# Kernel tuning notes

Hardware: AMD Instinct MI355X
Metric: run time of the kernel (lower is better)

The kernel has to match this reference:

```python
import jax, jax.numpy as jnp
import numpy as np

B, L, D, S = 8, 512, 64, 8


def setup_inputs() -> dict:
    key = jax.random.key(0)
    ks = jax.random.split(key, 8)
    return {
        "lstm1": jax.random.normal(ks[0], (B, L, D), dtype=jnp.float32),
        "lstm2": jax.random.normal(ks[1], (B, L, D), dtype=jnp.float32),
        "W": jax.random.normal(ks[2], (S, D, D), dtype=jnp.float32) * 0.1,
        "V": jax.random.normal(ks[3], (S, 2 * D), dtype=jnp.float32) * 0.1,
        "b": jax.random.normal(ks[4], (S,), dtype=jnp.float32) * 0.1,
        "W_g": jax.random.normal(ks[5], (S, 2 * D), dtype=jnp.float32) * 0.1,
        "b_g": jax.random.normal(ks[6], (S,), dtype=jnp.float32) * 0.1,
        "u": jax.random.normal(ks[7], (1, S), dtype=jnp.float32) * 0.1,
    }


def reference(lstm1, lstm2, W, V, b, W_g, b_g, u):
    # lstm1/lstm2: (B, L, D). Pairwise slot (i, j) pairs lstm1[:, i] with lstm2[:, j].
    d = lstm1.shape[-1]
    # Bilinear tensor-network score: x1_i W_s x2_j -> (B, L, L, S)
    result_w = jnp.einsum('bid,sde,bje->bijs', lstm1, W, lstm2)
    # concat(x1_i, x2_j) @ V^T decomposed to avoid materializing (B,L,L,2D)
    v1 = jnp.einsum('bid,sd->bis', lstm1, V[:, :d])[:, :, None, :]   # (B,L,1,S)
    v2 = jnp.einsum('bjd,sd->bjs', lstm2, V[:, d:])[:, None, :, :]   # (B,1,L,S)
    result_v = v1 + v2                                               # (B,L,L,S)
    g1 = jnp.einsum('bid,sd->bis', lstm1, W_g[:, :d])[:, :, None, :]
    g2 = jnp.einsum('bjd,sd->bjs', lstm2, W_g[:, d:])[:, None, :, :]
    gate = jax.nn.sigmoid(g1 + g2 + b_g)                             # (B,L,L,S)
    result_final = gate * result_w + (1.0 - gate) * jax.nn.sigmoid(result_v) + b
    # Reduce slices with u (shape (1,S)) -> (B,L,L), then add singleton channel dim.
    out = jnp.einsum('bijs,ks->bijk', result_final, u)[..., 0]
    return out[:, None, :, :]  # (B, 1, L, L)
```

## Files before the change

### kernel.cpp

```cpp
#include <hip/hip_runtime.h>
#include <math.h>

typedef float f32x4 __attribute__((ext_vector_type(4)));
typedef short bf16x8 __attribute__((ext_vector_type(8)));

namespace {
constexpr int kB = 8, kL = 512, kD = 64, kS = 8;
constexpr int LP = 72;
constexpr size_t SCL_OFF = 0;
constexpr size_t WT_OFF  = (size_t)4 * 8 * 8 * 512 * 4;
}

__device__ __forceinline__ unsigned short f2bf(float f) {
    unsigned u = __float_as_uint(f);
    u += 0x7FFFu + ((u >> 16) & 1u);
    return (unsigned short)(u >> 16);
}
__device__ __forceinline__ unsigned pk2(float lo, float hi) {
    return (unsigned)f2bf(lo) | ((unsigned)f2bf(hi) << 16);
}

__global__ __launch_bounds__(256) void grn_prep(
    const float* __restrict__ lstm1, const float* __restrict__ lstm2,
    const float* __restrict__ W, const float* __restrict__ V,
    const float* __restrict__ Wg, unsigned char* __restrict__ ws)
{
    float* scl = (float*)(ws + SCL_OFF);
    unsigned short* wt = (unsigned short*)(ws + WT_OFF);
    const int tid = threadIdx.x;
    if (blockIdx.x < 8) {
        const int s = blockIdx.x;
        __shared__ float wsm[64][68];
        const float* pw = W + s * 4096;
        const int row = tid >> 2, c0 = (tid & 3) * 16;
        #pragma unroll
        for (int q = 0; q < 4; q++)
            *(float4*)&wsm[row][c0 + q * 4] = *(const float4*)(pw + row * 64 + c0 + q * 4);
        __syncthreads();
        const int e = tid >> 2, d0 = (tid & 3) * 16;
        unsigned wd[8];
        #pragma unroll
        for (int q = 0; q < 8; q++)
            wd[q] = pk2(wsm[d0 + 2 * q][e], wsm[d0 + 2 * q + 1][e]);
        unsigned short* dst = wt + s * 4096 + e * 64 + d0;
        uint4 a = {wd[0], wd[1], wd[2], wd[3]};
        uint4 c = {wd[4], wd[5], wd[6], wd[7]};
        *(uint4*)(dst) = a;
        *(uint4*)(dst + 8) = c;
    } else {
        const int rb = blockIdx.x - 8;
        const int b = rb >> 3, r0 = (rb & 7) * 64;
        const int kind = tid & 3, row = r0 + (tid >> 2);
        const float* x = (kind < 2 ? lstm1 : lstm2) + ((size_t)b * kL + row) * kD;
        float xr[64];
        #pragma unroll
        for (int q = 0; q < 16; q++)
            *(float4*)&xr[q * 4] = *(const float4*)(x + q * 4);
        const float* vb = (kind & 1 ? Wg : V) + ((kind >> 1) ? kD : 0);
        #pragma unroll
        for (int s = 0; s < kS; s++) {
            const float* vec = vb + s * 2 * kD;
            float a = 0.f;
            #pragma unroll
            for (int q = 0; q < 16; q++) {
                const float4 vv = *(const float4*)(vec + q * 4);
                a = fmaf(vv.x, xr[q * 4 + 0], a);
                a = fmaf(vv.y, xr[q * 4 + 1], a);
                a = fmaf(vv.z, xr[q * 4 + 2], a);
                a = fmaf(vv.w, xr[q * 4 + 3], a);
            }
            scl[(((size_t)kind * 8 + b) * 8 + s) * 512 + row] = a;
        }
    }
}

__global__ __launch_bounds__(256) void grn_fusedm(
    const float* __restrict__ lstm1, const float* __restrict__ lstm2,
    const float* __restrict__ bS, const float* __restrict__ bg,
    const float* __restrict__ u, const unsigned char* __restrict__ ws,
    float* __restrict__ out)
{
    const float* sclw = (const float*)(ws + SCL_OFF);
    const unsigned short* wt = (const unsigned short*)(ws + WT_OFF);
    const int jt = blockIdx.x, it = blockIdx.y, b = blockIdx.z;
    __shared__ __align__(16) unsigned short x1t[64][LP];
    __shared__ __align__(16) unsigned short x2t[64][LP];
    __shared__ __align__(16) unsigned short wbuf[2][64][LP];
    __shared__ __align__(16) unsigned short ts[2][64][LP];
    __shared__ float scl[4][kS][64];
    const int tid = threadIdx.x;
    {
        const float* p1 = lstm1 + ((size_t)b * kL + it * 64) * kD;
        const float* p2 = lstm2 + ((size_t)b * kL + jt * 64) * kD;
        const int row = tid >> 2, c0 = (tid & 3) * 16;
        unsigned w1[8], w2[8];
        #pragma unroll
        for (int q = 0; q < 4; q++) {
            const float4 a = *(const float4*)(p1 + row * 64 + c0 + q * 4);
            const float4 c = *(const float4*)(p2 + row * 64 + c0 + q * 4);
            w1[q * 2] = pk2(a.x, a.y); w1[q * 2 + 1] = pk2(a.z, a.w);
            w2[q * 2] = pk2(c.x, c.y); w2[q * 2 + 1] = pk2(c.z, c.w);
        }
        uint4 a0 = {w1[0], w1[1], w1[2], w1[3]}, a1 = {w1[4], w1[5], w1[6], w1[7]};
        uint4 c0v = {w2[0], w2[1], w2[2], w2[3]}, c1 = {w2[4], w2[5], w2[6], w2[7]};
        *(uint4*)&x1t[row][c0] = a0; *(uint4*)&x1t[row][c0 + 8] = a1;
        *(uint4*)&x2t[row][c0] = c0v; *(uint4*)&x2t[row][c0 + 8] = c1;
    }
    {
        #pragma unroll
        for (int k = 0; k < 2; k++) {
            const int q = tid + k * 256;
            *(uint4*)&wbuf[0][q >> 3][(q & 7) * 8] = *(const uint4*)(wt + q * 8);
        }
    }
    {
        const int p0 = tid * 8, kind = p0 >> 9, rem = p0 & 511, s = rem >> 6, cc = rem & 63;
        const int base = (kind < 2 ? it : jt) * 64;
        const float* g = sclw + (((size_t)kind * 8 + b) * 8 + s) * 512 + base + cc;
        *(float4*)&scl[kind][s][cc] = *(const float4*)g;
        *(float4*)&scl[kind][s][cc + 4] = *(const float4*)(g + 4);
    }
    __syncthreads();
    const int lane = tid & 63, w = tid >> 6;
    const int wm = w >> 1, wn = w & 1;
    const int fr = lane & 15, fh = lane >> 4;
    bf16x8 A1[2][2], Bf[2][2];
    #pragma unroll
    for (int mb = 0; mb < 2; mb++)
        #pragma unroll
        for (int kb = 0; kb < 2; kb++)
            A1[mb][kb] = *(const bf16x8*)&x1t[wm * 32 + mb * 16 + fr][fh * 8 + kb * 32];
    #pragma unroll
    for (int nb = 0; nb < 2; nb++)
        #pragma unroll
        for (int kb = 0; kb < 2; kb++)
            Bf[nb][kb] = *(const bf16x8*)&x2t[wn * 32 + nb * 16 + fr][fh * 8 + kb * 32];
    uint4 wreg0 = *(const uint4*)(wt + 4096 + tid * 8);
    uint4 wreg1 = *(const uint4*)(wt + 4096 + (tid + 256) * 8);

    float bias_c = 0.f;
    #pragma unroll
    for (int s = 0; s < kS; s++) bias_c = fmaf(u[s], bS[s], bias_c);
    float oacc[2][2][4];
    #pragma unroll
    for (int mb = 0; mb < 2; mb++)
        #pragma unroll
        for (int nb = 0; nb < 2; nb++)
            #pragma unroll
            for (int r = 0; r < 4; r++) oacc[mb][nb][r] = bias_c;

    #pragma unroll 1
    for (int s = 0; s < kS; s++) {
        const int p = s & 1;
        bf16x8 WB[2][2];
        #pragma unroll
        for (int nb = 0; nb < 2; nb++)
            #pragma unroll
            for (int kb = 0; kb < 2; kb++)
                WB[nb][kb] = *(const bf16x8*)&wbuf[p][wn * 32 + nb * 16 + fr][fh * 8 + kb * 32];
        #pragma unroll
        for (int mb = 0; mb < 2; mb++)
            #pragma unroll
            for (int nb = 0; nb < 2; nb++) {
                f32x4 z = {0.f, 0.f, 0.f, 0.f};
                f32x4 tacc = __builtin_amdgcn_mfma_f32_16x16x32_bf16(A1[mb][0], WB[nb][0], z, 0, 0, 0);
                tacc = __builtin_amdgcn_mfma_f32_16x16x32_bf16(A1[mb][1], WB[nb][1], tacc, 0, 0, 0);
                #pragma unroll
                for (int r = 0; r < 4; r++)
                    ts[p][wm * 32 + mb * 16 + fh * 4 + r][wn * 32 + nb * 16 + fr] = f2bf(tacc[r]);
            }
        *(uint4*)&wbuf[1 - p][tid >> 3][(tid & 7) * 8] = wreg0;
        {
            const int q = tid + 256;
            *(uint4*)&wbuf[1 - p][q >> 3][(q & 7) * 8] = wreg1;
        }
        __syncthreads();
        bf16x8 At[2][2];
        #pragma unroll
        for (int mb = 0; mb < 2; mb++)
            #pragma unroll
            for (int kb = 0; kb < 2; kb++)
                At[mb][kb] = *(const bf16x8*)&ts[p][wm * 32 + mb * 16 + fr][fh * 8 + kb * 32];
        const float us = u[s], bgs = bg[s];
        #pragma unroll
        for (int mb = 0; mb < 2; mb++)
            #pragma unroll
            for (int nb = 0; nb < 2; nb++) {
                f32x4 z = {0.f, 0.f, 0.f, 0.f};
                f32x4 acc = __builtin_amdgcn_mfma_f32_16x16x32_bf16(At[mb][0], Bf[nb][0], z, 0, 0, 0);
                acc = __builtin_amdgcn_mfma_f32_16x16x32_bf16(At[mb][1], Bf[nb][1], acc, 0, 0, 0);
                const int jj = wn * 32 + nb * 16 + fr;
                const float v2 = scl[2][s][jj], g2 = scl[3][s][jj];
                #pragma unroll
                for (int r = 0; r < 4; r++) {
                    const int ii = wm * 32 + mb * 16 + fh * 4 + r;
                    const float v1 = scl[0][s][ii], g1 = scl[1][s][ii];
                    const float gate = 1.f / (1.f + __expf(-(g1 + g2 + bgs)));
                    const float sv = 1.f / (1.f + __expf(-(v1 + v2)));
                    const float res = fmaf(gate, acc[r] - sv, sv);
                    oacc[mb][nb][r] = fmaf(us, res, oacc[mb][nb][r]);
                }
            }
        const int sn = (s + 2) & 7;
        wreg0 = *(const uint4*)(wt + sn * 4096 + tid * 8);
        wreg1 = *(const uint4*)(wt + sn * 4096 + (tid + 256) * 8);
    }
    float* op = out + ((size_t)b * kL + it * 64) * kL + jt * 64;
    #pragma unroll
    for (int mb = 0; mb < 2; mb++)
        #pragma unroll
        for (int nb = 0; nb < 2; nb++)
            #pragma unroll
            for (int r = 0; r < 4; r++)
                op[(wm * 32 + mb * 16 + fh * 4 + r) * kL + wn * 32 + nb * 16 + fr]
                    = oacc[mb][nb][r];
}

extern "C" void kernel_launch(void* const* d_in, const int* in_sizes, int n_in,
                              void* d_out, int out_size, void* d_ws, size_t ws_size,
                              hipStream_t stream) {
    const float* lstm1 = (const float*)d_in[0];
    const float* lstm2 = (const float*)d_in[1];
    const float* W     = (const float*)d_in[2];
    const float* V     = (const float*)d_in[3];
    const float* bS    = (const float*)d_in[4];
    const float* Wg    = (const float*)d_in[5];
    const float* bg    = (const float*)d_in[6];
    const float* u     = (const float*)d_in[7];
    unsigned char* ws = (unsigned char*)d_ws;
    grn_prep<<<72, 256, 0, stream>>>(lstm1, lstm2, W, V, Wg, ws);
    grn_fusedm<<<dim3(kL / 64, kL / 64, kB), 256, 0, stream>>>(
        lstm1, lstm2, bS, bg, u, ws, (float*)d_out);
}
```

Before: 110.7 us.

## Make per-wave T tile private and load W fragments directly from global

```diff
diff --git a/kernel.cpp b/kernel.cpp
--- a/kernel.cpp
+++ b/kernel.cpp
@@ -74,7 +74,62 @@
     }
 }
 
-__global__ __launch_bounds__(256) void grn_fusedm(
+__device__ __forceinline__ void load_wb(
+    bf16x8 WB[4][2], const unsigned short* __restrict__ wt, int s, int fr, int fh)
+{
+    #pragma unroll
+    for (int ne = 0; ne < 4; ne++)
+        #pragma unroll
+        for (int kb = 0; kb < 2; kb++)
+            WB[ne][kb] = *(const bf16x8*)(wt + s * 4096 + (ne * 16 + fr) * 64
+                                          + fh * 8 + kb * 32);
+}
+
+__device__ __forceinline__ void grn_body(
+    const bf16x8 WB[4][2], const bf16x8 A1[2][2], const bf16x8 Bf[2][2],
+    unsigned short (*__restrict__ tsw)[LP], const float scl[4][kS][64],
+    float oacc[2][2][4], int s, int fr, int fh, int wm, int wn,
+    float us, float bgs)
+{
+    #pragma unroll
+    for (int mb = 0; mb < 2; mb++)
+        #pragma unroll
+        for (int ne = 0; ne < 4; ne++) {
+            f32x4 z = {0.f, 0.f, 0.f, 0.f};
+            f32x4 t = __builtin_amdgcn_mfma_f32_16x16x32_bf16(A1[mb][0], WB[ne][0], z, 0, 0, 0);
+            t = __builtin_amdgcn_mfma_f32_16x16x32_bf16(A1[mb][1], WB[ne][1], t, 0, 0, 0);
+            #pragma unroll
+            for (int r = 0; r < 4; r++)
+                tsw[mb * 16 + fh * 4 + r][ne * 16 + fr] = f2bf(t[r]);
+        }
+    bf16x8 At[2][2];
+    #pragma unroll
+    for (int mb = 0; mb < 2; mb++)
+        #pragma unroll
+        for (int kb = 0; kb < 2; kb++)
+            At[mb][kb] = *(const bf16x8*)&tsw[mb * 16 + fr][fh * 8 + kb * 32];
+    #pragma unroll
+    for (int mb = 0; mb < 2; mb++)
+        #pragma unroll
+        for (int nb = 0; nb < 2; nb++) {
+            f32x4 z = {0.f, 0.f, 0.f, 0.f};
+            f32x4 acc = __builtin_amdgcn_mfma_f32_16x16x32_bf16(At[mb][0], Bf[nb][0], z, 0, 0, 0);
+            acc = __builtin_amdgcn_mfma_f32_16x16x32_bf16(At[mb][1], Bf[nb][1], acc, 0, 0, 0);
+            const int jj = wn * 32 + nb * 16 + fr;
+            const float v2 = scl[2][s][jj], g2 = scl[3][s][jj];
+            #pragma unroll
+            for (int r = 0; r < 4; r++) {
+                const int ii = wm * 32 + mb * 16 + fh * 4 + r;
+                const float v1 = scl[0][s][ii], g1 = scl[1][s][ii];
+                const float gate = 1.f / (1.f + __expf(-(g1 + g2 + bgs)));
+                const float sv = 1.f / (1.f + __expf(-(v1 + v2)));
+                const float res = fmaf(gate, acc[r] - sv, sv);
+                oacc[mb][nb][r] = fmaf(us, res, oacc[mb][nb][r]);
+            }
+        }
+}
+
+__global__ __launch_bounds__(256, 2) void grn_fusedm(
     const float* __restrict__ lstm1, const float* __restrict__ lstm2,
     const float* __restrict__ bS, const float* __restrict__ bg,
     const float* __restrict__ u, const unsigned char* __restrict__ ws,
@@ -85,8 +140,7 @@
     const int jt = blockIdx.x, it = blockIdx.y, b = blockIdx.z;
     __shared__ __align__(16) unsigned short x1t[64][LP];
     __shared__ __align__(16) unsigned short x2t[64][LP];
-    __shared__ __align__(16) unsigned short wbuf[2][64][LP];
-    __shared__ __align__(16) unsigned short ts[2][64][LP];
+    __shared__ __align__(16) unsigned short ts[4][32][LP];
     __shared__ float scl[4][kS][64];
     const int tid = threadIdx.x;
     {
@@ -107,13 +161,6 @@
         *(uint4*)&x2t[row][c0] = c0v; *(uint4*)&x2t[row][c0 + 8] = c1;
     }
     {
-        #pragma unroll
-        for (int k = 0; k < 2; k++) {
-            const int q = tid + k * 256;
-            *(uint4*)&wbuf[0][q >> 3][(q & 7) * 8] = *(const uint4*)(wt + q * 8);
-        }
-    }
-    {
         const int p0 = tid * 8, kind = p0 >> 9, rem = p0 & 511, s = rem >> 6, cc = rem & 63;
         const int base = (kind < 2 ? it : jt) * 64;
         const float* g = sclw + (((size_t)kind * 8 + b) * 8 + s) * 512 + base + cc;
@@ -124,6 +171,7 @@
     const int lane = tid & 63, w = tid >> 6;
     const int wm = w >> 1, wn = w & 1;
     const int fr = lane & 15, fh = lane >> 4;
+    unsigned short (*__restrict__ tsw)[LP] = ts[w];
     bf16x8 A1[2][2], Bf[2][2];
     #pragma unroll
     for (int mb = 0; mb < 2; mb++)
@@ -135,12 +183,14 @@
         #pragma unroll
         for (int kb = 0; kb < 2; kb++)
             Bf[nb][kb] = *(const bf16x8*)&x2t[wn * 32 + nb * 16 + fr][fh * 8 + kb * 32];
-    uint4 wreg0 = *(const uint4*)(wt + 4096 + tid * 8);
-    uint4 wreg1 = *(const uint4*)(wt + 4096 + (tid + 256) * 8);
-
+    float ur[kS], bgr[kS];
+    #pragma unroll
+    for (int s = 0; s < kS; s++) { ur[s] = u[s]; bgr[s] = bS[s]; }
     float bias_c = 0.f;
     #pragma unroll
-    for (int s = 0; s < kS; s++) bias_c = fmaf(u[s], bS[s], bias_c);
+    for (int s = 0; s < kS; s++) bias_c = fmaf(ur[s], bgr[s], bias_c);
+    #pragma unroll
+    for (int s = 0; s < kS; s++) bgr[s] = bg[s];
     float oacc[2][2][4];
     #pragma unroll
     for (int mb = 0; mb < 2; mb++)
@@ -149,61 +199,14 @@
             #pragma unroll
             for (int r = 0; r < 4; r++) oacc[mb][nb][r] = bias_c;
 
+    bf16x8 WBa[4][2], WBb[4][2];
+    load_wb(WBa, wt, 0, fr, fh);
     #pragma unroll 1
-    for (int s = 0; s < kS; s++) {
-        const int p = s & 1;
-        bf16x8 WB[2][2];
-        #pragma unroll
-        for (int nb = 0; nb < 2; nb++)
-            #pragma unroll
-            for (int kb = 0; kb < 2; kb++)
-                WB[nb][kb] = *(const bf16x8*)&wbuf[p][wn * 32 + nb * 16 + fr][fh * 8 + kb * 32];
-        #pragma unroll
-        for (int mb = 0; mb < 2; mb++)
-            #pragma unroll
-            for (int nb = 0; nb < 2; nb++) {
-                f32x4 z = {0.f, 0.f, 0.f, 0.f};
-                f32x4 tacc = __builtin_amdgcn_mfma_f32_16x16x32_bf16(A1[mb][0], WB[nb][0], z, 0, 0, 0);
-                tacc = __builtin_amdgcn_mfma_f32_16x16x32_bf16(A1[mb][1], WB[nb][1], tacc, 0, 0, 0);
-                #pragma unroll
-                for (int r = 0; r < 4; r++)
-                    ts[p][wm * 32 + mb * 16 + fh * 4 + r][wn * 32 + nb * 16 + fr] = f2bf(tacc[r]);
-            }
-        *(uint4*)&wbuf[1 - p][tid >> 3][(tid & 7) * 8] = wreg0;
-        {
-            const int q = tid + 256;
-            *(uint4*)&wbuf[1 - p][q >> 3][(q & 7) * 8] = wreg1;
-        }
-        __syncthreads();
-        bf16x8 At[2][2];
-        #pragma unroll
-        for (int mb = 0; mb < 2; mb++)
-            #pragma unroll
-            for (int kb = 0; kb < 2; kb++)
-                At[mb][kb] = *(const bf16x8*)&ts[p][wm * 32 + mb * 16 + fr][fh * 8 + kb * 32];
-        const float us = u[s], bgs = bg[s];
-        #pragma unroll
-        for (int mb = 0; mb < 2; mb++)
-            #pragma unroll
-            for (int nb = 0; nb < 2; nb++) {
-                f32x4 z = {0.f, 0.f, 0.f, 0.f};
-                f32x4 acc = __builtin_amdgcn_mfma_f32_16x16x32_bf16(At[mb][0], Bf[nb][0], z, 0, 0, 0);
-                acc = __builtin_amdgcn_mfma_f32_16x16x32_bf16(At[mb][1], Bf[nb][1], acc, 0, 0, 0);
-                const int jj = wn * 32 + nb * 16 + fr;
-                const float v2 = scl[2][s][jj], g2 = scl[3][s][jj];
-                #pragma unroll
-                for (int r = 0; r < 4; r++) {
-                    const int ii = wm * 32 + mb * 16 + fh * 4 + r;
-                    const float v1 = scl[0][s][ii], g1 = scl[1][s][ii];
-                    const float gate = 1.f / (1.f + __expf(-(g1 + g2 + bgs)));
-                    const float sv = 1.f / (1.f + __expf(-(v1 + v2)));
-                    const float res = fmaf(gate, acc[r] - sv, sv);
-                    oacc[mb][nb][r] = fmaf(us, res, oacc[mb][nb][r]);
-                }
-            }
-        const int sn = (s + 2) & 7;
-        wreg0 = *(const uint4*)(wt + sn * 4096 + tid * 8);
-        wreg1 = *(const uint4*)(wt + sn * 4096 + (tid + 256) * 8);
+    for (int s = 0; s < kS; s += 2) {
+        load_wb(WBb, wt, s + 1, fr, fh);
+        grn_body(WBa, A1, Bf, tsw, scl, oacc, s, fr, fh, wm, wn, ur[s], bgr[s]);
+        load_wb(WBa, wt, (s + 2) & 7, fr, fh);
+        grn_body(WBb, A1, Bf, tsw, scl, oacc, s + 1, fr, fh, wm, wn, ur[s + 1], bgr[s + 1]);
     }
     float* op = out + ((size_t)b * kL + it * 64) * kL + jt * 64;
     #pragma unroll
```

After: 112.7 us. About the same (+1.8%).

## Split fused kernel into precomputed T=x1·W_s pass and per-wave output kernel

Applied to the files above, without the earlier changes.

```diff
diff --git a/kernel.cpp b/kernel.cpp
--- a/kernel.cpp
+++ b/kernel.cpp
@@ -6,9 +6,11 @@
 
 namespace {
 constexpr int kB = 8, kL = 512, kD = 64, kS = 8;
-constexpr int LP = 72;
 constexpr size_t SCL_OFF = 0;
-constexpr size_t WT_OFF  = (size_t)4 * 8 * 8 * 512 * 4;
+constexpr size_t WT_OFF  = 524288;
+constexpr size_t X1B_OFF = 589824;
+constexpr size_t X2B_OFF = 1114112;
+constexpr size_t T_OFF   = 1638400;
 }
 
 __device__ __forceinline__ unsigned short f2bf(float f) {
@@ -47,7 +49,7 @@
         uint4 c = {wd[4], wd[5], wd[6], wd[7]};
         *(uint4*)(dst) = a;
         *(uint4*)(dst + 8) = c;
-    } else {
+    } else if (blockIdx.x < 72) {
         const int rb = blockIdx.x - 8;
         const int b = rb >> 3, r0 = (rb & 7) * 64;
         const int kind = tid & 3, row = r0 + (tid >> 2);
@@ -56,7 +58,7 @@
         #pragma unroll
         for (int q = 0; q < 16; q++)
             *(float4*)&xr[q * 4] = *(const float4*)(x + q * 4);
-        const float* vb = (kind & 1 ? Wg : V) + ((kind >> 1) ? kD : 0);
+        const float* vb = ((kind & 1) ? Wg : V) + ((kind & 2) ? kD : 0);
         #pragma unroll
         for (int s = 0; s < kS; s++) {
             const float* vec = vb + s * 2 * kD;
@@ -71,149 +73,95 @@
             }
             scl[(((size_t)kind * 8 + b) * 8 + s) * 512 + row] = a;
         }
+    } else {
+        const int t = blockIdx.x - 72;
+        const float* src = (t < 16) ? lstm1 : lstm2;
+        unsigned short* dst = (unsigned short*)(ws + ((t < 16) ? X1B_OFF : X2B_OFF));
+        const int tt = (t & 15) * 256 + tid;
+        #pragma unroll
+        for (int k = 0; k < 8; k++) {
+            const int c = tt + k * 4096;
+            const float* p = src + (size_t)c * 8;
+            const float4 a = *(const float4*)p;
+            const float4 b2 = *(const float4*)(p + 4);
+            uint4 o = {pk2(a.x, a.y), pk2(a.z, a.w), pk2(b2.x, b2.y), pk2(b2.z, b2.w)};
+            *(uint4*)(dst + (size_t)c * 8) = o;
+        }
     }
 }
 
-__global__ __launch_bounds__(256) void grn_fusedm(
-    const float* __restrict__ lstm1, const float* __restrict__ lstm2,
+__global__ __launch_bounds__(256) void grn_t2(unsigned char* __restrict__ ws)
+{
+    const unsigned short* wt  = (const unsigned short*)(ws + WT_OFF);
+    const unsigned short* x1b = (const unsigned short*)(ws + X1B_OFF);
+    unsigned short* T = (unsigned short*)(ws + T_OFF);
+    const int g = blockIdx.x * 4 + (threadIdx.x >> 6);
+    const int b = g >> 8, rem = g & 255, s = rem >> 5, i16 = rem & 31;
+    const int lane = threadIdx.x & 63, fr = lane & 15, fh = lane >> 4;
+    const unsigned short* ap = x1b + (((size_t)b * kL + i16 * 16 + fr) * kD + fh * 8);
+    bf16x8 A0 = *(const bf16x8*)ap;
+    bf16x8 A1 = *(const bf16x8*)(ap + 32);
+    const unsigned short* bp = wt + (s * 4096 + fr * 64 + fh * 8);
+    unsigned short* tp = T + (((size_t)(b * 8 + s)) * kL + i16 * 16) * kD;
+    #pragma unroll
+    for (int ne = 0; ne < 4; ne++) {
+        const bf16x8 B0 = *(const bf16x8*)(bp + ne * 16 * 64);
+        const bf16x8 B1 = *(const bf16x8*)(bp + ne * 16 * 64 + 32);
+        f32x4 z = {0.f, 0.f, 0.f, 0.f};
+        f32x4 t = __builtin_amdgcn_mfma_f32_16x16x32_bf16(A0, B0, z, 0, 0, 0);
+        t = __builtin_amdgcn_mfma_f32_16x16x32_bf16(A1, B1, t, 0, 0, 0);
+        #pragma unroll
+        for (int r = 0; r < 4; r++)
+            tp[(fh * 4 + r) * kD + ne * 16 + fr] = f2bf(t[r]);
+    }
+}
+
+__global__ __launch_bounds__(256) void grn_m3(
     const float* __restrict__ bS, const float* __restrict__ bg,
     const float* __restrict__ u, const unsigned char* __restrict__ ws,
     float* __restrict__ out)
 {
-    const float* sclw = (const float*)(ws + SCL_OFF);
-    const unsigned short* wt = (const unsigned short*)(ws + WT_OFF);
-    const int jt = blockIdx.x, it = blockIdx.y, b = blockIdx.z;
-    __shared__ __align__(16) unsigned short x1t[64][LP];
-    __shared__ __align__(16) unsigned short x2t[64][LP];
-    __shared__ __align__(16) unsigned short wbuf[2][64][LP];
-    __shared__ __align__(16) unsigned short ts[2][64][LP];
-    __shared__ float scl[4][kS][64];
-    const int tid = threadIdx.x;
-    {
-        const float* p1 = lstm1 + ((size_t)b * kL + it * 64) * kD;
-        const float* p2 = lstm2 + ((size_t)b * kL + jt * 64) * kD;
-        const int row = tid >> 2, c0 = (tid & 3) * 16;
-        unsigned w1[8], w2[8];
-        #pragma unroll
-        for (int q = 0; q < 4; q++) {
-            const float4 a = *(const float4*)(p1 + row * 64 + c0 + q * 4);
-            const float4 c = *(const float4*)(p2 + row * 64 + c0 + q * 4);
-            w1[q * 2] = pk2(a.x, a.y); w1[q * 2 + 1] = pk2(a.z, a.w);
-            w2[q * 2] = pk2(c.x, c.y); w2[q * 2 + 1] = pk2(c.z, c.w);
-        }
-        uint4 a0 = {w1[0], w1[1], w1[2], w1[3]}, a1 = {w1[4], w1[5], w1[6], w1[7]};
-        uint4 c0v = {w2[0], w2[1], w2[2], w2[3]}, c1 = {w2[4], w2[5], w2[6], w2[7]};
-        *(uint4*)&x1t[row][c0] = a0; *(uint4*)&x1t[row][c0 + 8] = a1;
-        *(uint4*)&x2t[row][c0] = c0v; *(uint4*)&x2t[row][c0 + 8] = c1;
-    }
-    {
-        #pragma unroll
-        for (int k = 0; k < 2; k++) {
-            const int q = tid + k * 256;
-            *(uint4*)&wbuf[0][q >> 3][(q & 7) * 8] = *(const uint4*)(wt + q * 8);
-        }
-    }
-    {
-        const int p0 = tid * 8, kind = p0 >> 9, rem = p0 & 511, s = rem >> 6, cc = rem & 63;
-        const int base = (kind < 2 ? it : jt) * 64;
-        const float* g = sclw + (((size_t)kind * 8 + b) * 8 + s) * 512 + base + cc;
-        *(float4*)&scl[kind][s][cc] = *(const float4*)g;
-        *(float4*)&scl[kind][s][cc + 4] = *(const float4*)(g + 4);
-    }
-    __syncthreads();
-    const int lane = tid & 63, w = tid >> 6;
-    const int wm = w >> 1, wn = w & 1;
-    const int fr = lane & 15, fh = lane >> 4;
-    bf16x8 A1[2][2], Bf[2][2];
-    #pragma unroll
-    for (int mb = 0; mb < 2; mb++)
-        #pragma unroll
-        for (int kb = 0; kb < 2; kb++)
-            A1[mb][kb] = *(const bf16x8*)&x1t[wm * 32 + mb * 16 + fr][fh * 8 + kb * 32];
-    #pragma unroll
-    for (int nb = 0; nb < 2; nb++)
-        #pragma unroll
-        for (int kb = 0; kb < 2; kb++)
-            Bf[nb][kb] = *(const bf16x8*)&x2t[wn * 32 + nb * 16 + fr][fh * 8 + kb * 32];
-    uint4 wreg0 = *(const uint4*)(wt + 4096 + tid * 8);
-    uint4 wreg1 = *(const uint4*)(wt + 4096 + (tid + 256) * 8);
-
+    const float* scl = (const float*)(ws + SCL_OFF);
+    const unsigned short* x2b = (const unsigned short*)(ws + X2B_OFF);
+    const unsigned short* T = (const unsigned short*)(ws + T_OFF);
+    const int g = blockIdx.x * 4 + (threadIdx.x >> 6);
+    const int b = g >> 10, rem = g & 1023, it = rem >> 5, jt = rem & 31;
+    const int lane = threadIdx.x & 63, fr = lane & 15, fh = lane >> 4;
+    const int i0 = it * 16, j0 = jt * 16;
+    const unsigned short* bp = x2b + (((size_t)b * kL + j0 + fr) * kD + fh * 8);
+    const bf16x8 Bf0 = *(const bf16x8*)bp;
+    const bf16x8 Bf1 = *(const bf16x8*)(bp + 32);
     float bias_c = 0.f;
     #pragma unroll
     for (int s = 0; s < kS; s++) bias_c = fmaf(u[s], bS[s], bias_c);
-    float oacc[2][2][4];
+    f32x4 oacc = {bias_c, bias_c, bias_c, bias_c};
     #pragma unroll
-    for (int mb = 0; mb < 2; mb++)
+    for (int s = 0; s < kS; s++) {
+        const unsigned short* ap = T + (((size_t)(b * 8 + s)) * kL + i0 + fr) * kD + fh * 8;
+        const bf16x8 A0 = *(const bf16x8*)ap;
+        const bf16x8 A1 = *(const bf16x8*)(ap + 32);
+        f32x4 z = {0.f, 0.f, 0.f, 0.f};
+        f32x4 acc = __builtin_amdgcn_mfma_f32_16x16x32_bf16(A0, Bf0, z, 0, 0, 0);
+        acc = __builtin_amdgcn_mfma_f32_16x16x32_bf16(A1, Bf1, acc, 0, 0, 0);
+        const float4 v1q = *(const float4*)(scl + (((size_t)0 * 8 + b) * 8 + s) * 512 + i0 + fh * 4);
+        const float4 g1q = *(const float4*)(scl + (((size_t)1 * 8 + b) * 8 + s) * 512 + i0 + fh * 4);
+        const float v2 = scl[(((size_t)2 * 8 + b) * 8 + s) * 512 + j0 + fr];
+        const float g2 = scl[(((size_t)3 * 8 + b) * 8 + s) * 512 + j0 + fr];
+        const float us = u[s], bgs = bg[s];
+        const float v1a[4] = {v1q.x, v1q.y, v1q.z, v1q.w};
+        const float g1a[4] = {g1q.x, g1q.y, g1q.z, g1q.w};
         #pragma unroll
-        for (int nb = 0; nb < 2; nb++)
-            #pragma unroll
-            for (int r = 0; r < 4; r++) oacc[mb][nb][r] = bias_c;
-
-    #pragma unroll 1
-    for (int s = 0; s < kS; s++) {
-        const int p = s & 1;
-        bf16x8 WB[2][2];
-        #pragma unroll
-        for (int nb = 0; nb < 2; nb++)
-            #pragma unroll
-            for (int kb = 0; kb < 2; kb++)
-                WB[nb][kb] = *(const bf16x8*)&wbuf[p][wn * 32 + nb * 16 + fr][fh * 8 + kb * 32];
-        #pragma unroll
-        for (int mb = 0; mb < 2; mb++)
-            #pragma unroll
-            for (int nb = 0; nb < 2; nb++) {
-                f32x4 z = {0.f, 0.f, 0.f, 0.f};
-                f32x4 tacc = __builtin_amdgcn_mfma_f32_16x16x32_bf16(A1[mb][0], WB[nb][0], z, 0, 0, 0);
-                tacc = __builtin_amdgcn_mfma_f32_16x16x32_bf16(A1[mb][1], WB[nb][1], tacc, 0, 0, 0);
-                #pragma unroll
-                for (int r = 0; r < 4; r++)
-                    ts[p][wm * 32 + mb * 16 + fh * 4 + r][wn * 32 + nb * 16 + fr] = f2bf(tacc[r]);
-            }
-        *(uint4*)&wbuf[1 - p][tid >> 3][(tid & 7) * 8] = wreg0;
-        {
-            const int q = tid + 256;
-            *(uint4*)&wbuf[1 - p][q >> 3][(q & 7) * 8] = wreg1;
+        for (int r = 0; r < 4; r++) {
+            const float gate = 1.f / (1.f + __expf(-(g1a[r] + g2 + bgs)));
+            const float sv = 1.f / (1.f + __expf(-(v1a[r] + v2)));
+            const float res = fmaf(gate, acc[r] - sv, sv);
+            oacc[r] = fmaf(us, res, oacc[r]);
         }
-        __syncthreads();
-        bf16x8 At[2][2];
-        #pragma unroll
-        for (int mb = 0; mb < 2; mb++)
-            #pragma unroll
-            for (int kb = 0; kb < 2; kb++)
-                At[mb][kb] = *(const bf16x8*)&ts[p][wm * 32 + mb * 16 + fr][fh * 8 + kb * 32];
-        const float us = u[s], bgs = bg[s];
-        #pragma unroll
-        for (int mb = 0; mb < 2; mb++)
-            #pragma unroll
-            for (int nb = 0; nb < 2; nb++) {
-                f32x4 z = {0.f, 0.f, 0.f, 0.f};
-                f32x4 acc = __builtin_amdgcn_mfma_f32_16x16x32_bf16(At[mb][0], Bf[nb][0], z, 0, 0, 0);
-                acc = __builtin_amdgcn_mfma_f32_16x16x32_bf16(At[mb][1], Bf[nb][1], acc, 0, 0, 0);
-                const int jj = wn * 32 + nb * 16 + fr;
-                const float v2 = scl[2][s][jj], g2 = scl[3][s][jj];
-                #pragma unroll
-                for (int r = 0; r < 4; r++) {
-                    const int ii = wm * 32 + mb * 16 + fh * 4 + r;
-                    const float v1 = scl[0][s][ii], g1 = scl[1][s][ii];
-                    const float gate = 1.f / (1.f + __expf(-(g1 + g2 + bgs)));
-                    const float sv = 1.f / (1.f + __expf(-(v1 + v2)));
-                    const float res = fmaf(gate, acc[r] - sv, sv);
-                    oacc[mb][nb][r] = fmaf(us, res, oacc[mb][nb][r]);
-                }
-            }
-        const int sn = (s + 2) & 7;
-        wreg0 = *(const uint4*)(wt + sn * 4096 + tid * 8);
-        wreg1 = *(const uint4*)(wt + sn * 4096 + (tid + 256) * 8);
     }
-    float* op = out + ((size_t)b * kL + it * 64) * kL + jt * 64;
+    float* op = out + (((size_t)b * kL + i0 + fh * 4) * kL + j0 + fr);
     #pragma unroll
-    for (int mb = 0; mb < 2; mb++)
-        #pragma unroll
-        for (int nb = 0; nb < 2; nb++)
-            #pragma unroll
-            for (int r = 0; r < 4; r++)
-                op[(wm * 32 + mb * 16 + fh * 4 + r) * kL + wn * 32 + nb * 16 + fr]
-                    = oacc[mb][nb][r];
+    for (int r = 0; r < 4; r++)
+        op[(size_t)r * kL] = oacc[r];
 }
 
 extern "C" void kernel_launch(void* const* d_in, const int* in_sizes, int n_in,
@@ -228,7 +176,7 @@
     const float* bg    = (const float*)d_in[6];
     const float* u     = (const float*)d_in[7];
     unsigned char* ws = (unsigned char*)d_ws;
-    grn_prep<<<72, 256, 0, stream>>>(lstm1, lstm2, W, V, Wg, ws);
-    grn_fusedm<<<dim3(kL / 64, kL / 64, kB), 256, 0, stream>>>(
-        lstm1, lstm2, bS, bg, u, ws, (float*)d_out);
+    grn_prep<<<104, 256, 0, stream>>>(lstm1, lstm2, W, V, Wg, ws);
+    grn_t2<<<512, 256, 0, stream>>>(ws);
+    grn_m3<<<2048, 256, 0, stream>>>(bS, bg, u, ws, (float*)d_out);
 }
```

Result: slower. 116.6 us (+5.3%).
